# Kernel optimization log

Measured on AMD Instinct MI355X. Metric: run time of the kernel, lower is better.

## Reference

```python
import jax, jax.numpy as jnp
import numpy as np

DEPTH = 2          # number of transformer blocks
DIM = 1280         # hidden_size
NHEADS = 16
HDIM = DIM // NHEADS  # 80
FF = 5120          # intermediate_size
S = 8192           # total ragged tokens
NSEG = 8           # number of image segments
EPS = 1e-6
GRID = 32          # per-image patch grid side (32*32*8 = 8192)


def _rotate_half(x):
    h = x.shape[-1] // 2
    return jnp.concatenate([-x[..., h:], x[..., :h]], axis=-1)


def _layernorm(x, g, b):
    mu = jnp.mean(x, axis=-1, keepdims=True)
    var = jnp.mean(jnp.square(x - mu), axis=-1, keepdims=True)
    return (x - mu) * jax.lax.rsqrt(var + EPS) * g + b


def setup_inputs() -> dict:
    key = jax.random.key(0)
    ks = jax.random.split(key, 16)
    std = 0.02
    hidden_states = jax.random.normal(ks[0], (S, DIM), jnp.float32)
    cu_seqlens = jnp.arange(NSEG + 1, dtype=jnp.int32) * (S // NSEG)
    # 2D rotary: per-axis freq table of size head_dim//4, concat row+col -> head_dim//2,
    # duplicated (cat(freqs, freqs)) -> head_dim, then cos/sin.
    rot_dim = HDIM // 2
    inv_freq = 1.0 / (10000.0 ** (jnp.arange(0, rot_dim, 2, dtype=jnp.float32) / rot_dim))  # [HDIM//4]
    tok = jnp.arange(S)
    rows = ((tok % (GRID * GRID)) // GRID).astype(jnp.float32)
    cols = (tok % GRID).astype(jnp.float32)
    freqs = jnp.concatenate([rows[:, None] * inv_freq[None, :], cols[:, None] * inv_freq[None, :]], axis=-1)  # [S, HDIM//2]
    emb = jnp.concatenate([freqs, freqs], axis=-1)  # [S, HDIM]
    cos = jnp.cos(emb)
    sin = jnp.sin(emb)
    def rnd(k, shape):
        return jax.random.normal(k, shape, jnp.float32) * std
    params = {
        'ln1_g': jnp.ones((DEPTH, DIM), jnp.float32), 'ln1_b': jnp.zeros((DEPTH, DIM), jnp.float32),
        'ln2_g': jnp.ones((DEPTH, DIM), jnp.float32), 'ln2_b': jnp.zeros((DEPTH, DIM), jnp.float32),
        'qkv_w': rnd(ks[1], (DEPTH, 3 * DIM, DIM)), 'qkv_b': jnp.zeros((DEPTH, 3 * DIM), jnp.float32),
        'proj_w': rnd(ks[2], (DEPTH, DIM, DIM)), 'proj_b': jnp.zeros((DEPTH, DIM), jnp.float32),
        'fc1_w': rnd(ks[3], (DEPTH, FF, DIM)), 'fc1_b': jnp.zeros((DEPTH, FF), jnp.float32),
        'fc2_w': rnd(ks[4], (DEPTH, DIM, FF)), 'fc2_b': jnp.zeros((DEPTH, DIM), jnp.float32),
    }
    return dict(hidden_states=hidden_states, cu_seqlens=cu_seqlens, cos=cos, sin=sin, **params)


def reference(hidden_states, cu_seqlens, cos, sin,
              ln1_g, ln1_b, ln2_g, ln2_b,
              qkv_w, qkv_b, proj_w, proj_b,
              fc1_w, fc1_b, fc2_w, fc2_b):
    seq = hidden_states.shape[0]
    # cu_seqlens is a static (int) input; derive the block-diagonal segmentation.
    seg = np.diff(np.asarray(jax.device_get(cu_seqlens)))
    L = int(seg[0])
    assert (seg == L).all(), 'reference assumes equal-length segments'
    n = len(seg)
    scale = HDIM ** -0.5
    c = cos[:, None, :]  # broadcast over heads, like cos.unsqueeze(1)
    s_ = sin[:, None, :]
    x = hidden_states
    for i in range(DEPTH):
        # --- attention ---
        h = _layernorm(x, ln1_g[i], ln1_b[i])
        qkv = (h @ qkv_w[i].T + qkv_b[i]).reshape(seq, 3, NHEADS, HDIM)
        q, k, v = qkv[:, 0], qkv[:, 1], qkv[:, 2]
        q = q * c + _rotate_half(q) * s_
        k = k * c + _rotate_half(k) * s_
        qs = q.reshape(n, L, NHEADS, HDIM)
        ks_ = k.reshape(n, L, NHEADS, HDIM)
        vs = v.reshape(n, L, NHEADS, HDIM)
        # block-diagonal (per-segment) attention, fp32 softmax
        attn = jnp.einsum('nlhd,nkhd->nhlk', qs, ks_) * scale
        p = jax.nn.softmax(attn, axis=-1)
        o = jnp.einsum('nhlk,nkhd->nlhd', p, vs).reshape(seq, DIM)
        x = x + (o @ proj_w[i].T + proj_b[i])
        # --- mlp (gelu tanh approx) ---
        h2 = _layernorm(x, ln2_g[i], ln2_b[i])
        x = x + (jax.nn.gelu(h2 @ fc1_w[i].T + fc1_b[i], approximate=True) @ fc2_w[i].T + fc2_b[i])
    return x
```

## Files before the change

### kernel.cpp

```cpp
#include <hip/hip_runtime.h>
#include <hip/hip_bf16.h>

typedef __attribute__((ext_vector_type(8))) short bf16x8;
typedef __attribute__((ext_vector_type(4))) float f32x4;
typedef __attribute__((ext_vector_type(8))) unsigned short u16x8;
typedef __attribute__((ext_vector_type(4))) unsigned short u16x4;

__device__ __forceinline__ void gload_lds16(const void* g, void* l) {
  __builtin_amdgcn_global_load_lds(
      (const __attribute__((address_space(1))) unsigned int*)g,
      (__attribute__((address_space(3))) unsigned int*)l, 16, 0, 0);
}

__device__ __forceinline__ unsigned short f2bfu(float f) {
  __hip_bfloat16 h = __float2bfloat16(f);
  return __builtin_bit_cast(unsigned short, h);
}

__global__ __launch_bounds__(256) void copy_f32(const float* __restrict__ in,
                                                float* __restrict__ out, int n) {
  for (int i = blockIdx.x * 256 + threadIdx.x; i < n; i += gridDim.x * 256)
    out[i] = in[i];
}

__global__ __launch_bounds__(256) void w2bf(const float* __restrict__ in,
                                            __hip_bfloat16* __restrict__ out, int n) {
  for (int i = blockIdx.x * 256 + threadIdx.x; i < n; i += gridDim.x * 256)
    out[i] = __float2bfloat16(in[i]);
}

__global__ __launch_bounds__(256) void ln_kernel(const float* __restrict__ x,
                                                 const float* __restrict__ g,
                                                 const float* __restrict__ b,
                                                 __hip_bfloat16* __restrict__ h) {
  const int row = blockIdx.x;
  const int tid = threadIdx.x;
  const float* xr = x + (size_t)row * 1280;
  float v[5];
  float s = 0.f;
#pragma unroll
  for (int i = 0; i < 5; i++) { v[i] = xr[tid + i * 256]; s += v[i]; }
#pragma unroll
  for (int off = 32; off >= 1; off >>= 1) s += __shfl_xor(s, off);
  __shared__ float red[8];
  const int w = tid >> 6, lane = tid & 63;
  if (lane == 0) red[w] = s;
  __syncthreads();
  const float mu = (red[0] + red[1] + red[2] + red[3]) * (1.f / 1280.f);
  float q = 0.f;
#pragma unroll
  for (int i = 0; i < 5; i++) { float d = v[i] - mu; q += d * d; }
#pragma unroll
  for (int off = 32; off >= 1; off >>= 1) q += __shfl_xor(q, off);
  if (lane == 0) red[4 + w] = q;
  __syncthreads();
  const float var = (red[4] + red[5] + red[6] + red[7]) * (1.f / 1280.f);
  const float rstd = rsqrtf(var + 1e-6f);
#pragma unroll
  for (int i = 0; i < 5; i++) {
    int c = tid + i * 256;
    h[(size_t)row * 1280 + c] = __float2bfloat16((v[i] - mu) * rstd * g[c] + b[c]);
  }
}

__global__ __launch_bounds__(256) void rope_kernel(__hip_bfloat16* __restrict__ qkv,
                                                   const float* __restrict__ cs,
                                                   const float* __restrict__ sn) {
  const int TOT = 8192 * 2 * 16 * 40;
  for (int idx = blockIdx.x * 256 + threadIdx.x; idx < TOT; idx += gridDim.x * 256) {
    int d = idx % 40;
    int t = idx / 40;
    int head = t & 15;
    int t2 = t >> 4;
    int part = t2 & 1;
    int s = t2 >> 1;
    size_t base = ((size_t)s * 3 + part) * 1280 + head * 80;
    float e0 = __bfloat162float(qkv[base + d]);
    float e1 = __bfloat162float(qkv[base + d + 40]);
    float c0 = cs[s * 80 + d];
    float s0 = sn[s * 80 + d];
    float c1 = cs[s * 80 + d + 40];
    float s1 = sn[s * 80 + d + 40];
    qkv[base + d]      = __float2bfloat16(e0 * c0 - e1 * s0);
    qkv[base + d + 40] = __float2bfloat16(e1 * c1 + e0 * s1);
  }
}

__global__ __launch_bounds__(256) void vtrans_kernel(const __hip_bfloat16* __restrict__ qkv,
                                                     __hip_bfloat16* __restrict__ vt) {
  const int idx = blockIdx.x * 256 + threadIdx.x;
  const int s = idx & 8191;
  const int dc = idx >> 13;
  const unsigned short* src = (const unsigned short*)qkv + ((size_t)s * 3 + 2) * 1280 + dc * 8;
  u16x8 v = *(const u16x8*)src;
  unsigned short* dst = (unsigned short*)vt + (size_t)dc * 8 * 8192 + s;
#pragma unroll
  for (int j = 0; j < 8; j++) dst[(size_t)j * 8192] = v[j];
}

#define VMCNT4 asm volatile("s_waitcnt vmcnt(4)" ::: "memory")
#define VMCNT0 asm volatile("s_waitcnt vmcnt(0)" ::: "memory")

template <int EPI>
__global__ __launch_bounds__(512, 2) void gemm256(const __hip_bfloat16* __restrict__ A,
                                                  const __hip_bfloat16* __restrict__ B,
                                                  const float* __restrict__ bias,
                                                  __hip_bfloat16* __restrict__ C,
                                                  float* __restrict__ X,
                                                  int M, int N, int K) {
  __shared__ __align__(16) char lds[131072];
  const int tid = threadIdx.x, lane = tid & 63, w = tid >> 6;
  const int wr = w >> 2, wc = w & 3;
  const int lm = lane & 15, hi = lane >> 4;

  const int nby = M >> 8, nbx = N >> 8;
  const int xcd = blockIdx.x & 7;
  const int local = blockIdx.x >> 3;
  const int by = xcd * (nby >> 3) + local / nbx;
  const int bx = local % nbx;
  const long mBase = (long)by << 8, nBase = (long)bx << 8;

  f32x4 acc[8][4];
#pragma unroll
  for (int m = 0; m < 8; m++)
#pragma unroll
    for (int n = 0; n < 4; n++) acc[m][n] = (f32x4){0.f, 0.f, 0.f, 0.f};

  const int r0 = (w << 3) + (lane >> 3);
  const int slotT = (lane & 7) ^ (lane >> 3);
  const unsigned short* Ag = (const unsigned short*)A;
  const unsigned short* Bg = (const unsigned short*)B;
  const size_t aB = (size_t)(mBase + r0) * K + slotT * 8;
  const size_t bB = (size_t)(nBase + r0) * K + slotT * 8;
  const int wdst = w << 10;

  auto STAGE = [&](int tile, int half, int isB) {
    char* dst = lds + ((tile & 1) << 16) + (isB << 15) + (half << 14) + wdst;
    const unsigned short* src =
        (isB ? Bg + bB : Ag + aB) + (size_t)(half << 7) * (size_t)K + ((size_t)tile << 6);
    gload_lds16(src, dst);
    gload_lds16(src + ((size_t)K << 6), dst + 8192);
  };

  const int rowA = (wr * 64 + lm) * 128;
  const int rowB = (wc * 32 + lm) * 128 + 32768;
  const int key = lm & 7;
  int sw_s[2];
#pragma unroll
  for (int kk = 0; kk < 2; kk++) sw_s[kk] = (((kk << 2) | hi) ^ key) << 4;

  const int nt = K >> 6;

  STAGE(0, 0, 0); STAGE(0, 0, 1); STAGE(0, 1, 1); STAGE(0, 1, 0);
  STAGE(1, 0, 0); STAGE(1, 0, 1);
  VMCNT4;
  __builtin_amdgcn_s_barrier();

  for (int t = 0; t < nt; ++t) {
    const int bufOff = (t & 1) << 16;
    const bool s1 = t + 1 < nt, s2 = t + 2 < nt;
    bf16x8 af[4][2], bq[2][2][2];
#pragma unroll
    for (int mm = 0; mm < 4; mm++)
#pragma unroll
      for (int kk = 0; kk < 2; kk++)
        af[mm][kk] = *(const bf16x8*)(lds + bufOff + rowA + mm * 2048 + sw_s[kk]);
#pragma unroll
    for (int nh = 0; nh < 2; nh++)
#pragma unroll
      for (int nn = 0; nn < 2; nn++)
#pragma unroll
        for (int kk = 0; kk < 2; kk++)
          bq[nh][nn][kk] =
              *(const bf16x8*)(lds + bufOff + nh * 16384 + rowB + nn * 2048 + sw_s[kk]);
    if (s1) { STAGE(t + 1, 1, 1); STAGE(t + 1, 1, 0); }
    __builtin_amdgcn_s_barrier();
    __builtin_amdgcn_s_setprio(1);
#pragma unroll
    for (int kk = 0; kk < 2; kk++)
#pragma unroll
      for (int mm = 0; mm < 4; mm++)
#pragma unroll
        for (int n = 0; n < 4; n++)
          acc[mm][n] = __builtin_amdgcn_mfma_f32_16x16x32_bf16(
              af[mm][kk], bq[n >> 1][n & 1][kk], acc[mm][n], 0, 0, 0);
    __builtin_amdgcn_s_setprio(0);
    __builtin_amdgcn_s_barrier();
#pragma unroll
    for (int mm = 0; mm < 4; mm++)
#pragma unroll
      for (int kk = 0; kk < 2; kk++)
        af[mm][kk] = *(const bf16x8*)(lds + bufOff + 16384 + rowA + mm * 2048 + sw_s[kk]);
    if (s2) { STAGE(t + 2, 0, 0); STAGE(t + 2, 0, 1); }
    __builtin_amdgcn_s_barrier();
    __builtin_amdgcn_s_setprio(1);
#pragma unroll
    for (int kk = 0; kk < 2; kk++)
#pragma unroll
      for (int mm = 0; mm < 4; mm++)
#pragma unroll
        for (int n = 0; n < 4; n++)
          acc[4 + mm][n] = __builtin_amdgcn_mfma_f32_16x16x32_bf16(
              af[mm][kk], bq[n >> 1][n & 1][kk], acc[4 + mm][n], 0, 0, 0);
    __builtin_amdgcn_s_setprio(0);
    if (t == nt - 2) { VMCNT0; } else { VMCNT4; }
    __builtin_amdgcn_s_barrier();
  }

  float* eb = (float*)(lds + w * 9216);
  float bvv[2][2];
#pragma unroll
  for (int nh = 0; nh < 2; nh++)
#pragma unroll
    for (int nn = 0; nn < 2; nn++)
      bvv[nh][nn] = bias[nBase + nh * 128 + wc * 32 + nn * 16 + lm];

#pragma unroll
  for (int mh = 0; mh < 2; mh++)
#pragma unroll
    for (int nh = 0; nh < 2; nh++) {
#pragma unroll
      for (int mm = 0; mm < 4; mm++)
#pragma unroll
        for (int nn = 0; nn < 2; nn++)
#pragma unroll
          for (int j = 0; j < 4; j++)
            eb[(mm * 16 + hi * 4 + j) * 36 + nn * 16 + lm] =
                acc[mh * 4 + mm][nh * 2 + nn][j] + bvv[nh][nn];
#pragma unroll
      for (int rr = 0; rr < 8; rr++) {
        const int r = rr * 8 + (lane >> 3);
        const int c = (lane & 7) * 4;
        f32x4 v = *(const f32x4*)&eb[r * 36 + c];
        const int grow = (int)mBase + mh * 128 + wr * 64 + r;
        const int gcol = (int)nBase + nh * 128 + wc * 32 + c;
        const size_t off = (size_t)grow * N + gcol;
        if constexpr (EPI == 0) {
          u16x4 o4;
#pragma unroll
          for (int q = 0; q < 4; q++) o4[q] = f2bfu(v[q]);
          *(u16x4*)((__hip_bfloat16*)C + off) = o4;
        } else if constexpr (EPI == 1) {
          u16x4 o4;
#pragma unroll
          for (int q = 0; q < 4; q++) {
            float u = v[q] + 0.044715f * v[q] * v[q] * v[q];
            float E = exp2f(2.30220818f * u);
            float th = 1.f - 2.f / (E + 1.f);
            o4[q] = f2bfu(0.5f * v[q] * (1.f + th));
          }
          *(u16x4*)((__hip_bfloat16*)C + off) = o4;
        } else {
          f32x4 x = *(const f32x4*)&X[off];
          x += v;
          *(f32x4*)&X[off] = x;
        }
      }
    }
}

__global__ __launch_bounds__(512, 4) void attn_kernel(const __hip_bfloat16* __restrict__ qkv,
                                                      const __hip_bfloat16* __restrict__ vtg,
                                                      __hip_bfloat16* __restrict__ o) {
  __shared__ __align__(16) unsigned short Ks[128 * 96];
  __shared__ __align__(16) unsigned short Vt[80 * 136];
  __shared__ __align__(16) unsigned short Ps[8][16 * 68];
  const int tid = threadIdx.x, lane = tid & 63, w = tid >> 6;
  const int lm = lane & 15, hi = lane >> 4;
  const int qt = blockIdx.x, head = blockIdx.y, seg = blockIdx.z;
  const int s0 = seg * 1024;
  const int qrow0 = s0 + qt * 128;
  const unsigned short* qg = (const unsigned short*)qkv;
  const unsigned short* vg = (const unsigned short*)vtg + (size_t)head * 80 * 8192;

  for (int idx = tid; idx < 2048; idx += 512) {
    int r = idx >> 4, c = 80 + (idx & 15);
    Ks[r * 96 + c] = 0;
  }

  bf16x8 aq[3];
  {
    const unsigned short* qrow = qg + (size_t)(qrow0 + w * 16 + lm) * 3840 + head * 80;
#pragma unroll
    for (int kk = 0; kk < 3; kk++) aq[kk] = *(const bf16x8*)(qrow + kk * 32 + hi * 8);
  }

  auto loadKV = [&](int kt, u16x8* kr, u16x8* vr) {
#pragma unroll
    for (int it = 0; it < 3; it++) {
      int c = tid + it * 512;
      if (c < 1280) {
        int r = c / 10, c8 = c % 10;
        kr[it] = *(const u16x8*)(qg + ((size_t)(s0 + kt * 128 + r) * 3 + 1) * 1280 +
                                 head * 80 + c8 * 8);
        int d = c >> 4, sc = c & 15;
        vr[it] = *(const u16x8*)(vg + (size_t)d * 8192 + s0 + kt * 128 + sc * 8);
      }
    }
  };
  auto writeKV = [&](u16x8* kr, u16x8* vr) {
#pragma unroll
    for (int it = 0; it < 3; it++) {
      int c = tid + it * 512;
      if (c < 1280) {
        int r = c / 10, c8 = c % 10;
        *(u16x8*)&Ks[r * 96 + c8 * 8] = kr[it];
        int d = c >> 4, sc = c & 15;
        *(u16x8*)&Vt[d * 136 + sc * 8] = vr[it];
      }
    }
  };

  {
    u16x8 kr[3], vr[3];
    loadKV(0, kr, vr);
    writeKV(kr, vr);
  }
  __syncthreads();

  float m_s[4] = {-1e30f, -1e30f, -1e30f, -1e30f};
  float l_s[4] = {0.f, 0.f, 0.f, 0.f};
  f32x4 accO[5];
#pragma unroll
  for (int nf = 0; nf < 5; nf++) accO[nf] = (f32x4){0.f, 0.f, 0.f, 0.f};

  const float SM = 0.11180339887498949f * 1.4426950408889634f;

  for (int kt = 0; kt < 8; kt++) {
    u16x8 krn[3], vrn[3];
    if (kt + 1 < 8) loadKV(kt + 1, krn, vrn);

    f32x4 sf[8];
#pragma unroll
    for (int n = 0; n < 8; n++) sf[n] = (f32x4){0.f, 0.f, 0.f, 0.f};
    __builtin_amdgcn_s_setprio(1);
#pragma unroll
    for (int kk = 0; kk < 3; kk++) {
#pragma unroll
      for (int n = 0; n < 8; n++) {
        bf16x8 bk = *(const bf16x8*)(&Ks[(n * 16 + lm) * 96 + kk * 32 + hi * 8]);
        sf[n] = __builtin_amdgcn_mfma_f32_16x16x32_bf16(aq[kk], bk, sf[n], 0, 0, 0);
      }
    }
    __builtin_amdgcn_s_setprio(0);

    float vmax[4];
    float growth = -1e30f;
#pragma unroll
    for (int j = 0; j < 4; j++) {
      float v = sf[0][j];
#pragma unroll
      for (int n = 1; n < 8; n++) v = fmaxf(v, sf[n][j]);
#pragma unroll
      for (int off = 1; off < 16; off <<= 1) v = fmaxf(v, __shfl_xor(v, off));
      vmax[j] = v;
      growth = fmaxf(growth, (v - m_s[j]) * SM);
    }
    if (__any(growth > 12.0f)) {
#pragma unroll
      for (int j = 0; j < 4; j++) {
        float mn = fmaxf(m_s[j], vmax[j]);
        float alpha = exp2f((m_s[j] - mn) * SM);
        m_s[j] = mn;
        l_s[j] *= alpha;
#pragma unroll
        for (int nf = 0; nf < 5; nf++) accO[nf][j] *= alpha;
      }
    }
    float rsum[4] = {0.f, 0.f, 0.f, 0.f};
#pragma unroll
    for (int n = 0; n < 8; n++)
#pragma unroll
      for (int j = 0; j < 4; j++) {
        float p = exp2f((sf[n][j] - m_s[j]) * SM);
        sf[n][j] = p;
        rsum[j] += p;
      }
#pragma unroll
    for (int j = 0; j < 4; j++) {
#pragma unroll
      for (int off = 1; off < 16; off <<= 1) rsum[j] += __shfl_xor(rsum[j], off);
      l_s[j] += rsum[j];
    }

#pragma unroll
    for (int h = 0; h < 2; h++) {
#pragma unroll
      for (int n = 0; n < 4; n++)
#pragma unroll
        for (int j = 0; j < 4; j++)
          Ps[w][(hi * 4 + j) * 68 + n * 16 + lm] = f2bfu(sf[h * 4 + n][j]);
      __builtin_amdgcn_s_setprio(1);
#pragma unroll
      for (int kk = 0; kk < 2; kk++) {
        bf16x8 pa = *(const bf16x8*)(&Ps[w][lm * 68 + kk * 32 + hi * 8]);
#pragma unroll
        for (int nf = 0; nf < 5; nf++) {
          bf16x8 bv =
              *(const bf16x8*)(&Vt[(nf * 16 + lm) * 136 + h * 64 + kk * 32 + hi * 8]);
          accO[nf] = __builtin_amdgcn_mfma_f32_16x16x32_bf16(pa, bv, accO[nf], 0, 0, 0);
        }
      }
      __builtin_amdgcn_s_setprio(0);
    }

    __syncthreads();
    if (kt + 1 < 8) writeKV(krn, vrn);
    __syncthreads();
  }

#pragma unroll
  for (int nf = 0; nf < 5; nf++) {
    int d = nf * 16 + lm;
#pragma unroll
    for (int j = 0; j < 4; j++) {
      int r = qrow0 + w * 16 + hi * 4 + j;
      o[(size_t)r * 1280 + head * 80 + d] = __float2bfloat16(accO[nf][j] / l_s[j]);
    }
  }
}

extern "C" void kernel_launch(void* const* d_in, const int* in_sizes, int n_in,
                              void* d_out, int out_size, void* d_ws, size_t ws_size,
                              hipStream_t stream) {
  (void)in_sizes; (void)n_in; (void)out_size; (void)ws_size;
  const float* hidden = (const float*)d_in[0];
  const float* cs   = (const float*)d_in[2];
  const float* sn   = (const float*)d_in[3];
  const float* ln1g = (const float*)d_in[4];
  const float* ln1b = (const float*)d_in[5];
  const float* ln2g = (const float*)d_in[6];
  const float* ln2b = (const float*)d_in[7];
  const float* qkvw = (const float*)d_in[8];
  const float* qkvb = (const float*)d_in[9];
  const float* pw   = (const float*)d_in[10];
  const float* pb   = (const float*)d_in[11];
  const float* f1w  = (const float*)d_in[12];
  const float* f1b  = (const float*)d_in[13];
  const float* f2w  = (const float*)d_in[14];
  const float* f2b  = (const float*)d_in[15];

  float* x = (float*)d_out;

  char* ws = (char*)d_ws;
  __hip_bfloat16* h    = (__hip_bfloat16*)ws;
  __hip_bfloat16* vt   = (__hip_bfloat16*)ws;
  __hip_bfloat16* qkv  = (__hip_bfloat16*)(ws + 20971520);
  __hip_bfloat16* o    = (__hip_bfloat16*)(ws + 83886080);
  __hip_bfloat16* ffh  = (__hip_bfloat16*)(ws + 20971520);
  __hip_bfloat16* wbuf = (__hip_bfloat16*)(ws + 104857600);

  const int NTOK = 8192 * 1280;
  copy_f32<<<2048, 256, 0, stream>>>(hidden, x, NTOK);
  for (int i = 0; i < 2; i++) {
    ln_kernel<<<8192, 256, 0, stream>>>(x, ln1g + i * 1280, ln1b + i * 1280, h);

    w2bf<<<2048, 256, 0, stream>>>(qkvw + (size_t)i * 3840 * 1280, wbuf, 3840 * 1280);
    gemm256<0><<<480, 512, 0, stream>>>(h, wbuf, qkvb + i * 3840, qkv, nullptr,
                                        8192, 3840, 1280);
    vtrans_kernel<<<5120, 256, 0, stream>>>(qkv, vt);
    rope_kernel<<<4096, 256, 0, stream>>>(qkv, cs, sn);
    attn_kernel<<<dim3(8, 16, 8), 512, 0, stream>>>(qkv, vt, o);

    w2bf<<<2048, 256, 0, stream>>>(pw + (size_t)i * 1280 * 1280, wbuf, 1280 * 1280);
    gemm256<2><<<160, 512, 0, stream>>>(o, wbuf, pb + i * 1280, nullptr, x,
                                        8192, 1280, 1280);

    ln_kernel<<<8192, 256, 0, stream>>>(x, ln2g + i * 1280, ln2b + i * 1280, h);

    w2bf<<<2048, 256, 0, stream>>>(f1w + (size_t)i * 5120 * 1280, wbuf, 5120 * 1280);
    gemm256<1><<<640, 512, 0, stream>>>(h, wbuf, f1b + i * 5120, ffh, nullptr,
                                        8192, 5120, 1280);

    w2bf<<<2048, 256, 0, stream>>>(f2w + (size_t)i * 1280 * 5120, wbuf, 1280 * 5120);
    gemm256<2><<<160, 512, 0, stream>>>(ffh, wbuf, f2b + i * 1280, nullptr, x,
                                        8192, 1280, 5120);
  }
}
```

Before: 1.283 ms.

## Drop hidden-state copy and merge GEMM half-step barriers into one phase

The initial copy of hidden_states into the output buffer is removed. The first layernorm now reads the input directly, and a new GEMM epilogue variant (EPI 3) adds the original hidden states into the output after the first projection. Inside the GEMM main loop, both A half-tiles and the B fragments are now read from LDS up front, so both next-stage prefetches can be issued after a single barrier. This removes one barrier pair per K-step. The cost is more live registers for the extra A fragments, which could add register pressure at two waves per SIMD.

```diff
diff --git a/kernel.cpp b/kernel.cpp
--- a/kernel.cpp
+++ b/kernel.cpp
@@ -15,12 +15,6 @@
 __device__ __forceinline__ unsigned short f2bfu(float f) {
   __hip_bfloat16 h = __float2bfloat16(f);
   return __builtin_bit_cast(unsigned short, h);
-}
-
-__global__ __launch_bounds__(256) void copy_f32(const float* __restrict__ in,
-                                                float* __restrict__ out, int n) {
-  for (int i = blockIdx.x * 256 + threadIdx.x; i < n; i += gridDim.x * 256)
-    out[i] = in[i];
 }
 
 __global__ __launch_bounds__(256) void w2bf(const float* __restrict__ in,
@@ -107,6 +101,7 @@
                                                   const float* __restrict__ bias,
                                                   __hip_bfloat16* __restrict__ C,
                                                   float* __restrict__ X,
+                                                  const float* __restrict__ H,
                                                   int M, int N, int K) {
   __shared__ __align__(16) char lds[131072];
   const int tid = threadIdx.x, lane = tid & 63, w = tid >> 6;
@@ -159,7 +154,7 @@
   for (int t = 0; t < nt; ++t) {
     const int bufOff = (t & 1) << 16;
     const bool s1 = t + 1 < nt, s2 = t + 2 < nt;
-    bf16x8 af[4][2], bq[2][2][2];
+    bf16x8 af[4][2], ag[4][2], bq[2][2][2];
 #pragma unroll
     for (int mm = 0; mm < 4; mm++)
 #pragma unroll
@@ -173,8 +168,14 @@
         for (int kk = 0; kk < 2; kk++)
           bq[nh][nn][kk] =
               *(const bf16x8*)(lds + bufOff + nh * 16384 + rowB + nn * 2048 + sw_s[kk]);
+#pragma unroll
+    for (int mm = 0; mm < 4; mm++)
+#pragma unroll
+      for (int kk = 0; kk < 2; kk++)
+        ag[mm][kk] = *(const bf16x8*)(lds + bufOff + 16384 + rowA + mm * 2048 + sw_s[kk]);
     if (s1) { STAGE(t + 1, 1, 1); STAGE(t + 1, 1, 0); }
     __builtin_amdgcn_s_barrier();
+    if (s2) { STAGE(t + 2, 0, 0); STAGE(t + 2, 0, 1); }
     __builtin_amdgcn_s_setprio(1);
 #pragma unroll
     for (int kk = 0; kk < 2; kk++)
@@ -184,16 +185,6 @@
         for (int n = 0; n < 4; n++)
           acc[mm][n] = __builtin_amdgcn_mfma_f32_16x16x32_bf16(
               af[mm][kk], bq[n >> 1][n & 1][kk], acc[mm][n], 0, 0, 0);
-    __builtin_amdgcn_s_setprio(0);
-    __builtin_amdgcn_s_barrier();
-#pragma unroll
-    for (int mm = 0; mm < 4; mm++)
-#pragma unroll
-      for (int kk = 0; kk < 2; kk++)
-        af[mm][kk] = *(const bf16x8*)(lds + bufOff + 16384 + rowA + mm * 2048 + sw_s[kk]);
-    if (s2) { STAGE(t + 2, 0, 0); STAGE(t + 2, 0, 1); }
-    __builtin_amdgcn_s_barrier();
-    __builtin_amdgcn_s_setprio(1);
 #pragma unroll
     for (int kk = 0; kk < 2; kk++)
 #pragma unroll
@@ -201,7 +192,7 @@
 #pragma unroll
         for (int n = 0; n < 4; n++)
           acc[4 + mm][n] = __builtin_amdgcn_mfma_f32_16x16x32_bf16(
-              af[mm][kk], bq[n >> 1][n & 1][kk], acc[4 + mm][n], 0, 0, 0);
+              ag[mm][kk], bq[n >> 1][n & 1][kk], acc[4 + mm][n], 0, 0, 0);
     __builtin_amdgcn_s_setprio(0);
     if (t == nt - 2) { VMCNT0; } else { VMCNT4; }
     __builtin_amdgcn_s_barrier();
@@ -250,8 +241,12 @@
             o4[q] = f2bfu(0.5f * v[q] * (1.f + th));
           }
           *(u16x4*)((__hip_bfloat16*)C + off) = o4;
+        } else if constexpr (EPI == 2) {
+          f32x4 x = *(const f32x4*)&X[off];
+          x += v;
+          *(f32x4*)&X[off] = x;
         } else {
-          f32x4 x = *(const f32x4*)&X[off];
+          f32x4 x = *(const f32x4*)&H[off];
           x += v;
           *(f32x4*)&X[off] = x;
         }
@@ -450,30 +445,33 @@
   __hip_bfloat16* ffh  = (__hip_bfloat16*)(ws + 20971520);
   __hip_bfloat16* wbuf = (__hip_bfloat16*)(ws + 104857600);
 
-  const int NTOK = 8192 * 1280;
-  copy_f32<<<2048, 256, 0, stream>>>(hidden, x, NTOK);
   for (int i = 0; i < 2; i++) {
-    ln_kernel<<<8192, 256, 0, stream>>>(x, ln1g + i * 1280, ln1b + i * 1280, h);
+    ln_kernel<<<8192, 256, 0, stream>>>(i == 0 ? hidden : x, ln1g + i * 1280,
+                                        ln1b + i * 1280, h);
 
     w2bf<<<2048, 256, 0, stream>>>(qkvw + (size_t)i * 3840 * 1280, wbuf, 3840 * 1280);
-    gemm256<0><<<480, 512, 0, stream>>>(h, wbuf, qkvb + i * 3840, qkv, nullptr,
+    gemm256<0><<<480, 512, 0, stream>>>(h, wbuf, qkvb + i * 3840, qkv, nullptr, nullptr,
                                         8192, 3840, 1280);
     vtrans_kernel<<<5120, 256, 0, stream>>>(qkv, vt);
     rope_kernel<<<4096, 256, 0, stream>>>(qkv, cs, sn);
     attn_kernel<<<dim3(8, 16, 8), 512, 0, stream>>>(qkv, vt, o);
 
     w2bf<<<2048, 256, 0, stream>>>(pw + (size_t)i * 1280 * 1280, wbuf, 1280 * 1280);
-    gemm256<2><<<160, 512, 0, stream>>>(o, wbuf, pb + i * 1280, nullptr, x,
-                                        8192, 1280, 1280);
+    if (i == 0)
+      gemm256<3><<<160, 512, 0, stream>>>(o, wbuf, pb, nullptr, x, hidden,
+                                          8192, 1280, 1280);
+    else
+      gemm256<2><<<160, 512, 0, stream>>>(o, wbuf, pb + 1280, nullptr, x, nullptr,
+                                          8192, 1280, 1280);
 
     ln_kernel<<<8192, 256, 0, stream>>>(x, ln2g + i * 1280, ln2b + i * 1280, h);
 
     w2bf<<<2048, 256, 0, stream>>>(f1w + (size_t)i * 5120 * 1280, wbuf, 5120 * 1280);
-    gemm256<1><<<640, 512, 0, stream>>>(h, wbuf, f1b + i * 5120, ffh, nullptr,
+    gemm256<1><<<640, 512, 0, stream>>>(h, wbuf, f1b + i * 5120, ffh, nullptr, nullptr,
                                         8192, 5120, 1280);
 
     w2bf<<<2048, 256, 0, stream>>>(f2w + (size_t)i * 1280 * 5120, wbuf, 1280 * 5120);
-    gemm256<2><<<160, 512, 0, stream>>>(ffh, wbuf, f2b + i * 1280, nullptr, x,
+    gemm256<2><<<160, 512, 0, stream>>>(ffh, wbuf, f2b + i * 1280, nullptr, x, nullptr,
                                         8192, 1280, 5120);
   }
 }
```

Measured after the change: 1.278 ms (median of 2 runs). About the same (-0.4%).
